# Kernel optimization log

Hardware: AMD Instinct MI355X
Metric: run time of the kernel (lower is better)

## Reference

```python
import jax, jax.numpy as jnp
import numpy as np

N_STEPS = 100
TAU_S = 5.0  # network_config['tau_s']
SHAPE = (16, 128, 16, 16, N_STEPS)  # [B, C, H, W, T]


def psp(target):
    """Leaky-integrator postsynaptic potential: syn_t = syn_{t-1}*(1-1/tau_s) + x_t, emit syn_t/tau_s."""
    x = jnp.moveaxis(target, -1, 0)  # time-major [T, B, C, H, W]
    decay = 1.0 - 1.0 / TAU_S

    def step(syn, xt):
        syn = syn * decay + xt
        return syn, syn / TAU_S

    _, syns = jax.lax.scan(step, jnp.zeros_like(x[0]), x)
    return jnp.moveaxis(syns, 0, -1)  # back to [B, C, H, W, T]


def setup_inputs() -> dict:
    key = jax.random.key(0)
    k1, k2 = jax.random.split(key)
    outputs = jax.random.normal(k1, SHAPE, dtype=jnp.float32) * 0.1
    target = (jax.random.uniform(k2, SHAPE) < 0.2).astype(jnp.float32)
    return {"outputs": outputs, "target": target}


def reference(outputs, target):
    # SpikeLoss.spike_kernel: 0.5 * sum((outputs - psp(target))**2)
    delta = outputs - psp(target)
    return 0.5 * jnp.sum(delta ** 2)
```

## Files before the change

### kernel.cpp

```cpp
#include <hip/hip_runtime.h>


#define T_STEPS 100
#define SEG 25
#define NPB 64
#define BLOCK 256
#define N_NEURONS (16 * 128 * 16 * 16)
#define GRID_P (N_NEURONS / NPB)
#define F4_PER_ARR (NPB * T_STEPS / 4)

#define GLOBAL_AS __attribute__((address_space(1)))
#define LDS_AS __attribute__((address_space(3)))

__device__ __forceinline__ void async_f4(const float4* g, float4* l) {
  __builtin_amdgcn_global_load_lds((const GLOBAL_AS void*)g, (LDS_AS void*)l,
                                   16, 0, 0);
}

__device__ __forceinline__ float block_loss(const float* __restrict__ outputs,
                                            const float* __restrict__ target) {
  __shared__ float xbuf[NPB * T_STEPS];
  __shared__ float obuf[NPB * T_STEPS];
  __shared__ float lE[NPB * 4];
  __shared__ float wsum[BLOCK / 64];

  const int tid = threadIdx.x;
  const size_t base = (size_t)blockIdx.x * (NPB * T_STEPS);
  const float4* gt = reinterpret_cast<const float4*>(target + base);
  const float4* go = reinterpret_cast<const float4*>(outputs + base);
  float4* lx4 = reinterpret_cast<float4*>(xbuf);
  float4* lo4 = reinterpret_cast<float4*>(obuf);

#pragma unroll
  for (int it = 0; it < 6; ++it) async_f4(gt + it * 256 + tid, lx4 + it * 256 + tid);
  if (tid < F4_PER_ARR - 1536) async_f4(gt + 1536 + tid, lx4 + 1536 + tid);
#pragma unroll
  for (int it = 0; it < 6; ++it) async_f4(go + it * 256 + tid, lo4 + it * 256 + tid);
  if (tid < F4_PER_ARR - 1536) async_f4(go + 1536 + tid, lo4 + 1536 + tid);

  __syncthreads();

  const int n = tid >> 2;
  const int s = tid & 3;
  const float* xrow = xbuf + n * T_STEPS + s * SEG;
  float E = 0.f;
#pragma unroll
  for (int j = 0; j < SEG; ++j) E = fmaf(E, 0.8f, xrow[j]);
  lE[tid] = E;

  __syncthreads();

  const float A25 = 3.77789319e-3f;
  const float A50 = 1.42724769e-5f;
  float carry = 0.f;
  if (s >= 1) carry = lE[tid - 1];
  if (s >= 2) carry = fmaf(A25, lE[tid - 2], carry);
  if (s >= 3) carry = fmaf(A50, lE[tid - 3], carry);

  const float* orow = obuf + n * T_STEPS + s * SEG;
  float syn = carry;
  float acc = 0.f;
#pragma unroll
  for (int j = 0; j < SEG; ++j) {
    syn = fmaf(syn, 0.8f, xrow[j]);
    float d = fmaf(-0.2f, syn, orow[j]);
    acc = fmaf(d, d, acc);
  }

#pragma unroll
  for (int off = 32; off > 0; off >>= 1) acc += __shfl_down(acc, off, 64);
  const int lane = tid & 63;
  const int wid = tid >> 6;
  if (lane == 0) wsum[wid] = acc;
  __syncthreads();
  return wsum[0] + wsum[1] + wsum[2] + wsum[3];
}

__global__ __launch_bounds__(BLOCK, 3) void spike_loss_partial(
    const float* __restrict__ outputs,
    const float* __restrict__ target,
    float* __restrict__ partial) {
  float blocksum = block_loss(outputs, target);
  if (threadIdx.x == 0) partial[blockIdx.x] = blocksum;
}

__global__ __launch_bounds__(256) void spike_loss_final(
    const float* __restrict__ partial, float* __restrict__ out, int nparts) {
  float acc = 0.0f;
  for (int i = threadIdx.x; i < nparts; i += 256) acc += partial[i];
#pragma unroll
  for (int off = 32; off > 0; off >>= 1) acc += __shfl_down(acc, off, 64);
  __shared__ float wsum[4];
  const int lane = threadIdx.x & 63;
  const int wid = threadIdx.x >> 6;
  if (lane == 0) wsum[wid] = acc;
  __syncthreads();
  if (threadIdx.x == 0) out[0] = 0.5f * (wsum[0] + wsum[1] + wsum[2] + wsum[3]);
}

__global__ __launch_bounds__(BLOCK, 3) void spike_loss_atomic(
    const float* __restrict__ outputs,
    const float* __restrict__ target,
    float* __restrict__ out) {
  float blocksum = block_loss(outputs, target);
  if (threadIdx.x == 0) atomicAdd(out, 0.5f * blocksum);
}

extern "C" void kernel_launch(void* const* d_in, const int* in_sizes, int n_in,
                              void* d_out, int out_size, void* d_ws, size_t ws_size,
                              hipStream_t stream) {
  const float* outputs = (const float*)d_in[0];
  const float* target = (const float*)d_in[1];
  float* out = (float*)d_out;

  if (ws_size >= GRID_P * sizeof(float)) {
    float* partial = (float*)d_ws;
    spike_loss_partial<<<GRID_P, BLOCK, 0, stream>>>(outputs, target, partial);
    spike_loss_final<<<1, 256, 0, stream>>>(partial, out, GRID_P);
  } else {
    hipMemsetAsync(out, 0, sizeof(float), stream);
    spike_loss_atomic<<<GRID_P, BLOCK, 0, stream>>>(outputs, target, out);
  }
}
```

Baseline: 409.5 us.

## Make blocks persistent over several chunks with double-buffered async LDS loads

Each block shrinks to 128 threads and walks 8 chunks of 32 neurons instead of loading one 64-neuron tile. The loads for the next chunk go into a second LDS buffer through global_load_lds while the current chunk is computed, with explicit vmcnt waits and barriers. This aims to hide global memory latency inside each block rather than relying on many resident blocks. It cuts the grid size and adds more barriers per chunk, and the hand-written vmcnt(14) count must match the number of loads issued for correctness.

```diff
diff --git a/kernel.cpp b/kernel.cpp
--- a/kernel.cpp
+++ b/kernel.cpp
@@ -3,11 +3,14 @@
 
 #define T_STEPS 100
 #define SEG 25
-#define NPB 64
-#define BLOCK 256
+#define NPC 32
+#define BLOCK 128
+#define CPB 8
+#define CHUNK_FLOATS (NPC * T_STEPS)
 #define N_NEURONS (16 * 128 * 16 * 16)
-#define GRID_P (N_NEURONS / NPB)
-#define F4_PER_ARR (NPB * T_STEPS / 4)
+#define TOTAL_CHUNKS (N_NEURONS / NPC)
+#define GRID_P (TOTAL_CHUNKS / CPB)
+#define NPARTS (N_NEURONS / 64)
 
 #define GLOBAL_AS __attribute__((address_space(1)))
 #define LDS_AS __attribute__((address_space(3)))
@@ -16,72 +19,117 @@
   __builtin_amdgcn_global_load_lds((const GLOBAL_AS void*)g, (LDS_AS void*)l,
                                    16, 0, 0);
 }
+__device__ __forceinline__ void async_f1(const float* g, float* l) {
+  __builtin_amdgcn_global_load_lds((const GLOBAL_AS void*)g, (LDS_AS void*)l,
+                                   4, 0, 0);
+}
 
-__device__ __forceinline__ float block_loss(const float* __restrict__ outputs,
-                                            const float* __restrict__ target) {
-  __shared__ float xbuf[NPB * T_STEPS];
-  __shared__ float obuf[NPB * T_STEPS];
-  __shared__ float lE[NPB * 4];
-  __shared__ float wsum[BLOCK / 64];
+__device__ __forceinline__ void issue_chunk(const float* gx, const float* go,
+                                            float* lx, float* lo, int tid) {
+  const float4* gx4 = reinterpret_cast<const float4*>(gx);
+  const float4* go4 = reinterpret_cast<const float4*>(go);
+  float4* lx4 = reinterpret_cast<float4*>(lx);
+  float4* lo4 = reinterpret_cast<float4*>(lo);
+#pragma unroll
+  for (int it = 0; it < 6; ++it)
+    async_f4(gx4 + it * BLOCK + tid, lx4 + it * BLOCK + tid);
+  async_f1(gx + 6 * BLOCK * 4 + tid, lx + 6 * BLOCK * 4 + tid);
+#pragma unroll
+  for (int it = 0; it < 6; ++it)
+    async_f4(go4 + it * BLOCK + tid, lo4 + it * BLOCK + tid);
+  async_f1(go + 6 * BLOCK * 4 + tid, lo + 6 * BLOCK * 4 + tid);
+}
+
+template <bool WRITE_PARTIAL>
+__device__ __forceinline__ void block_body(const float* __restrict__ outputs,
+                                           const float* __restrict__ target,
+                                           float* __restrict__ partial,
+                                           float* __restrict__ out) {
+  __shared__ float xbuf[2][CHUNK_FLOATS];
+  __shared__ float obuf[2][CHUNK_FLOATS];
+  __shared__ float lE[BLOCK];
+  __shared__ float ws2[2][2];
 
   const int tid = threadIdx.x;
-  const size_t base = (size_t)blockIdx.x * (NPB * T_STEPS);
-  const float4* gt = reinterpret_cast<const float4*>(target + base);
-  const float4* go = reinterpret_cast<const float4*>(outputs + base);
-  float4* lx4 = reinterpret_cast<float4*>(xbuf);
-  float4* lo4 = reinterpret_cast<float4*>(obuf);
+  const size_t base = (size_t)blockIdx.x * (CPB * CHUNK_FLOATS);
+  const float* tg = target + base;
+  const float* og = outputs + base;
 
-#pragma unroll
-  for (int it = 0; it < 6; ++it) async_f4(gt + it * 256 + tid, lx4 + it * 256 + tid);
-  if (tid < F4_PER_ARR - 1536) async_f4(gt + 1536 + tid, lx4 + 1536 + tid);
-#pragma unroll
-  for (int it = 0; it < 6; ++it) async_f4(go + it * 256 + tid, lo4 + it * 256 + tid);
-  if (tid < F4_PER_ARR - 1536) async_f4(go + 1536 + tid, lo4 + 1536 + tid);
-
-  __syncthreads();
+  issue_chunk(tg, og, xbuf[0], obuf[0], tid);
 
   const int n = tid >> 2;
   const int s = tid & 3;
-  const float* xrow = xbuf + n * T_STEPS + s * SEG;
-  float E = 0.f;
-#pragma unroll
-  for (int j = 0; j < SEG; ++j) E = fmaf(E, 0.8f, xrow[j]);
-  lE[tid] = E;
-
-  __syncthreads();
-
   const float A25 = 3.77789319e-3f;
   const float A50 = 1.42724769e-5f;
-  float carry = 0.f;
-  if (s >= 1) carry = lE[tid - 1];
-  if (s >= 2) carry = fmaf(A25, lE[tid - 2], carry);
-  if (s >= 3) carry = fmaf(A50, lE[tid - 3], carry);
+  float bsum = 0.f;
 
-  const float* orow = obuf + n * T_STEPS + s * SEG;
-  float syn = carry;
-  float acc = 0.f;
+  for (int k = 0; k < CPB; ++k) {
+    const int cur = k & 1;
+
+    if (k + 1 < CPB) {
+      issue_chunk(tg + (size_t)(k + 1) * CHUNK_FLOATS,
+                  og + (size_t)(k + 1) * CHUNK_FLOATS,
+                  xbuf[cur ^ 1], obuf[cur ^ 1], tid);
+      asm volatile("s_waitcnt vmcnt(14)" ::: "memory");
+    } else {
+      asm volatile("s_waitcnt vmcnt(0)" ::: "memory");
+    }
+    __builtin_amdgcn_sched_barrier(0);
+    __builtin_amdgcn_s_barrier();
+    __builtin_amdgcn_sched_barrier(0);
+
+    const float* xrow = &xbuf[cur][n * T_STEPS + s * SEG];
+    const float* orow = &obuf[cur][n * T_STEPS + s * SEG];
+
+    float E = 0.f;
 #pragma unroll
-  for (int j = 0; j < SEG; ++j) {
-    syn = fmaf(syn, 0.8f, xrow[j]);
-    float d = fmaf(-0.2f, syn, orow[j]);
-    acc = fmaf(d, d, acc);
+    for (int j = 0; j < SEG; ++j) E = fmaf(E, 0.8f, xrow[j]);
+    lE[tid] = E;
+    asm volatile("s_waitcnt lgkmcnt(0)" ::: "memory");
+    __builtin_amdgcn_s_barrier();
+    __builtin_amdgcn_sched_barrier(0);
+
+    float carry = 0.f;
+    if (s >= 1) carry = lE[tid - 1];
+    if (s >= 2) carry = fmaf(A25, lE[tid - 2], carry);
+    if (s >= 3) carry = fmaf(A50, lE[tid - 3], carry);
+
+    float syn = carry;
+    float acc = 0.f;
+#pragma unroll
+    for (int j = 0; j < SEG; ++j) {
+      syn = fmaf(syn, 0.8f, xrow[j]);
+      float d = fmaf(-0.2f, syn, orow[j]);
+      acc = fmaf(d, d, acc);
+    }
+
+#pragma unroll
+    for (int off = 32; off > 0; off >>= 1) acc += __shfl_down(acc, off, 64);
+    if ((tid & 63) == 0) ws2[cur][tid >> 6] = acc;
+
+    asm volatile("s_waitcnt lgkmcnt(0)" ::: "memory");
+    __builtin_amdgcn_sched_barrier(0);
+    __builtin_amdgcn_s_barrier();
+    __builtin_amdgcn_sched_barrier(0);
+
+    if (cur == 1 && tid == 0) {
+      float g = ((ws2[0][0] + ws2[0][1]) + ws2[1][0]) + ws2[1][1];
+      if (WRITE_PARTIAL) {
+        partial[(size_t)blockIdx.x * (CPB / 2) + (k >> 1)] = g;
+      } else {
+        bsum += g;
+      }
+    }
   }
 
-#pragma unroll
-  for (int off = 32; off > 0; off >>= 1) acc += __shfl_down(acc, off, 64);
-  const int lane = tid & 63;
-  const int wid = tid >> 6;
-  if (lane == 0) wsum[wid] = acc;
-  __syncthreads();
-  return wsum[0] + wsum[1] + wsum[2] + wsum[3];
+  if (!WRITE_PARTIAL && tid == 0) atomicAdd(out, 0.5f * bsum);
 }
 
-__global__ __launch_bounds__(BLOCK, 3) void spike_loss_partial(
+__global__ __launch_bounds__(BLOCK) void spike_loss_partial(
     const float* __restrict__ outputs,
     const float* __restrict__ target,
     float* __restrict__ partial) {
-  float blocksum = block_loss(outputs, target);
-  if (threadIdx.x == 0) partial[blockIdx.x] = blocksum;
+  block_body<true>(outputs, target, partial, nullptr);
 }
 
 __global__ __launch_bounds__(256) void spike_loss_final(
@@ -98,12 +146,11 @@
   if (threadIdx.x == 0) out[0] = 0.5f * (wsum[0] + wsum[1] + wsum[2] + wsum[3]);
 }
 
-__global__ __launch_bounds__(BLOCK, 3) void spike_loss_atomic(
+__global__ __launch_bounds__(BLOCK) void spike_loss_atomic(
     const float* __restrict__ outputs,
     const float* __restrict__ target,
     float* __restrict__ out) {
-  float blocksum = block_loss(outputs, target);
-  if (threadIdx.x == 0) atomicAdd(out, 0.5f * blocksum);
+  block_body<false>(outputs, target, nullptr, out);
 }
 
 extern "C" void kernel_launch(void* const* d_in, const int* in_sizes, int n_in,
@@ -113,10 +160,10 @@
   const float* target = (const float*)d_in[1];
   float* out = (float*)d_out;
 
-  if (ws_size >= GRID_P * sizeof(float)) {
+  if (ws_size >= NPARTS * sizeof(float)) {
     float* partial = (float*)d_ws;
     spike_loss_partial<<<GRID_P, BLOCK, 0, stream>>>(outputs, target, partial);
-    spike_loss_final<<<1, 256, 0, stream>>>(partial, out, GRID_P);
+    spike_loss_final<<<1, 256, 0, stream>>>(partial, out, NPARTS);
   } else {
     hipMemsetAsync(out, 0, sizeof(float), stream);
     spike_loss_atomic<<<GRID_P, BLOCK, 0, stream>>>(outputs, target, out);
```

Measured after the change: 419.1 us. 2.3% more time.

## Reuse one LDS buffer for target and outputs to double occupancy

Applied to the files above, without the earlier changes.

The kernel now stages the target tile into LDS, copies each thread's 25-step segment into registers, and then reuses the same LDS buffer for the outputs tile. This halves LDS use per block, so launch bounds go from 3 to 6 blocks per CU. The segment-carry exchange moves from an LDS array to width-4 shuffles. Staging the two tiles one after the other puts the outputs load after the first sync, which may expose latency that was overlapped before, and the register array adds register pressure.

```diff
diff --git a/kernel.cpp b/kernel.cpp
--- a/kernel.cpp
+++ b/kernel.cpp
@@ -7,7 +7,8 @@
 #define BLOCK 256
 #define N_NEURONS (16 * 128 * 16 * 16)
 #define GRID_P (N_NEURONS / NPB)
-#define F4_PER_ARR (NPB * T_STEPS / 4)
+#define NPARTS GRID_P
+#define BLK_FLOATS (NPB * T_STEPS)
 
 #define GLOBAL_AS __attribute__((address_space(1)))
 #define LDS_AS __attribute__((address_space(3)))
@@ -16,54 +17,67 @@
   __builtin_amdgcn_global_load_lds((const GLOBAL_AS void*)g, (LDS_AS void*)l,
                                    16, 0, 0);
 }
+__device__ __forceinline__ void async_f1(const float* g, float* l) {
+  __builtin_amdgcn_global_load_lds((const GLOBAL_AS void*)g, (LDS_AS void*)l,
+                                   4, 0, 0);
+}
 
-__device__ __forceinline__ float block_loss(const float* __restrict__ outputs,
-                                            const float* __restrict__ target) {
-  __shared__ float xbuf[NPB * T_STEPS];
-  __shared__ float obuf[NPB * T_STEPS];
-  __shared__ float lE[NPB * 4];
+__device__ __forceinline__ void stage(const float* __restrict__ g,
+                                      float* lds, int tid) {
+  const float4* g4 = reinterpret_cast<const float4*>(g);
+  float4* l4 = reinterpret_cast<float4*>(lds);
+#pragma unroll
+  for (int it = 0; it < 6; ++it)
+    async_f4(g4 + it * BLOCK + tid, l4 + it * BLOCK + tid);
+  async_f1(g + 6 * BLOCK * 4 + tid, lds + 6 * BLOCK * 4 + tid);
+}
+
+template <bool WRITE_PARTIAL>
+__device__ __forceinline__ void block_body(const float* __restrict__ outputs,
+                                           const float* __restrict__ target,
+                                           float* __restrict__ partial,
+                                           float* __restrict__ out) {
+  __shared__ float buf[BLK_FLOATS];
   __shared__ float wsum[BLOCK / 64];
 
   const int tid = threadIdx.x;
-  const size_t base = (size_t)blockIdx.x * (NPB * T_STEPS);
-  const float4* gt = reinterpret_cast<const float4*>(target + base);
-  const float4* go = reinterpret_cast<const float4*>(outputs + base);
-  float4* lx4 = reinterpret_cast<float4*>(xbuf);
-  float4* lo4 = reinterpret_cast<float4*>(obuf);
+  const size_t base = (size_t)blockIdx.x * BLK_FLOATS;
 
+  stage(target + base, buf, tid);
+  __syncthreads();
+
+  const int s = tid & 3;
+  const int rowoff = tid * SEG;
+  float xr[SEG];
 #pragma unroll
-  for (int it = 0; it < 6; ++it) async_f4(gt + it * 256 + tid, lx4 + it * 256 + tid);
-  if (tid < F4_PER_ARR - 1536) async_f4(gt + 1536 + tid, lx4 + 1536 + tid);
-#pragma unroll
-  for (int it = 0; it < 6; ++it) async_f4(go + it * 256 + tid, lo4 + it * 256 + tid);
-  if (tid < F4_PER_ARR - 1536) async_f4(go + 1536 + tid, lo4 + 1536 + tid);
+  for (int j = 0; j < SEG; ++j) xr[j] = buf[rowoff + j];
 
   __syncthreads();
 
-  const int n = tid >> 2;
-  const int s = tid & 3;
-  const float* xrow = xbuf + n * T_STEPS + s * SEG;
+  stage(outputs + base, buf, tid);
+
   float E = 0.f;
 #pragma unroll
-  for (int j = 0; j < SEG; ++j) E = fmaf(E, 0.8f, xrow[j]);
-  lE[tid] = E;
+  for (int j = 0; j < SEG; ++j) E = fmaf(E, 0.8f, xr[j]);
+
+  const float A25 = 3.77789319e-3f;
+  const float A50 = 1.42724769e-5f;
+  const float e1 = __shfl_up(E, 1, 4);
+  const float e2 = __shfl_up(E, 2, 4);
+  const float e3 = __shfl_up(E, 3, 4);
+  float carry = 0.f;
+  if (s >= 1) carry = e1;
+  if (s >= 2) carry = fmaf(A25, e2, carry);
+  if (s >= 3) carry = fmaf(A50, e3, carry);
 
   __syncthreads();
 
-  const float A25 = 3.77789319e-3f;
-  const float A50 = 1.42724769e-5f;
-  float carry = 0.f;
-  if (s >= 1) carry = lE[tid - 1];
-  if (s >= 2) carry = fmaf(A25, lE[tid - 2], carry);
-  if (s >= 3) carry = fmaf(A50, lE[tid - 3], carry);
-
-  const float* orow = obuf + n * T_STEPS + s * SEG;
   float syn = carry;
   float acc = 0.f;
 #pragma unroll
   for (int j = 0; j < SEG; ++j) {
-    syn = fmaf(syn, 0.8f, xrow[j]);
-    float d = fmaf(-0.2f, syn, orow[j]);
+    syn = fmaf(syn, 0.8f, xr[j]);
+    float d = fmaf(-0.2f, syn, buf[rowoff + j]);
     acc = fmaf(d, d, acc);
   }
 
@@ -73,15 +87,19 @@
   const int wid = tid >> 6;
   if (lane == 0) wsum[wid] = acc;
   __syncthreads();
-  return wsum[0] + wsum[1] + wsum[2] + wsum[3];
+  const float blocksum = ((wsum[0] + wsum[1]) + wsum[2]) + wsum[3];
+
+  if (tid == 0) {
+    if (WRITE_PARTIAL) partial[blockIdx.x] = blocksum;
+    else atomicAdd(out, 0.5f * blocksum);
+  }
 }
 
-__global__ __launch_bounds__(BLOCK, 3) void spike_loss_partial(
+__global__ __launch_bounds__(BLOCK, 6) void spike_loss_partial(
     const float* __restrict__ outputs,
     const float* __restrict__ target,
     float* __restrict__ partial) {
-  float blocksum = block_loss(outputs, target);
-  if (threadIdx.x == 0) partial[blockIdx.x] = blocksum;
+  block_body<true>(outputs, target, partial, nullptr);
 }
 
 __global__ __launch_bounds__(256) void spike_loss_final(
@@ -98,12 +116,11 @@
   if (threadIdx.x == 0) out[0] = 0.5f * (wsum[0] + wsum[1] + wsum[2] + wsum[3]);
 }
 
-__global__ __launch_bounds__(BLOCK, 3) void spike_loss_atomic(
+__global__ __launch_bounds__(BLOCK, 6) void spike_loss_atomic(
     const float* __restrict__ outputs,
     const float* __restrict__ target,
     float* __restrict__ out) {
-  float blocksum = block_loss(outputs, target);
-  if (threadIdx.x == 0) atomicAdd(out, 0.5f * blocksum);
+  block_body<false>(outputs, target, nullptr, out);
 }
 
 extern "C" void kernel_launch(void* const* d_in, const int* in_sizes, int n_in,
@@ -113,10 +130,10 @@
   const float* target = (const float*)d_in[1];
   float* out = (float*)d_out;
 
-  if (ws_size >= GRID_P * sizeof(float)) {
+  if (ws_size >= NPARTS * sizeof(float)) {
     float* partial = (float*)d_ws;
     spike_loss_partial<<<GRID_P, BLOCK, 0, stream>>>(outputs, target, partial);
-    spike_loss_final<<<1, 256, 0, stream>>>(partial, out, GRID_P);
+    spike_loss_final<<<1, 256, 0, stream>>>(partial, out, NPARTS);
   } else {
     hipMemsetAsync(out, 0, sizeof(float), stream);
     spike_loss_atomic<<<GRID_P, BLOCK, 0, stream>>>(outputs, target, out);
```

Result: no change. 407.9 us (-0.4%).
